# Kernel optimization log

Hardware: AMD Instinct MI355X
Metric: run time of the kernel (lower is better)

The kernel has to match this reference:

```python
import jax, jax.numpy as jnp
import numpy as np
from jax import lax

MIN_VALUE = 0.0
MAX_VALUE = 1.0

# 5-point Laplacian stencil kernel, OIHW layout
_LAP_KERNEL = jnp.array([[0.0, 1.0, 0.0],
                         [1.0, -4.0, 1.0],
                         [0.0, 1.0, 0.0]], dtype=jnp.float32).reshape(1, 1, 3, 3)


def _laplacian(u):
    # u: [B, 1, H, W], zero-padded 3x3 stencil (SAME)
    return lax.conv_general_dilated(
        u, _LAP_KERNEL, window_strides=(1, 1), padding='SAME',
        dimension_numbers=('NCHW', 'OIHW', 'NCHW'))


def _step(u, params):
    # Fisher-Kolmogorov reaction-diffusion step:
    #   diff = D * laplacian(u) + rho * u * (1 - u)
    D = params[:, 0:1]    # [B,1,H,W]
    rho = params[:, 1:2]  # [B,1,H,W]
    return D * _laplacian(u) + rho * u * (1.0 - u)


def setup_inputs() -> dict:
    key = jax.random.key(0)
    k1, k2, k3 = jax.random.split(key, 3)
    B, H, W = 32, 256, 256
    u = jax.random.uniform(k1, (B, 1, H, W), dtype=jnp.float32)
    params = jax.random.uniform(k2, (B, 2, H, W), dtype=jnp.float32)
    t = jax.random.randint(k3, (B,), 0, 32, dtype=jnp.int32)
    return {"u": u, "params": params, "t": t}


def reference(u, params, t):
    # Original: for step in range(max(t)): u[t>step] += step(u[t>step], params[t>step]); clip(u).
    # The step is per-sample local, so masked gather/scatter == predicated full update.
    max_duration = int(jnp.max(t))  # static trip count

    def body(step, u):
        mask = (t > step).astype(u.dtype)[:, None, None, None]  # [B,1,1,1]
        u = u + mask * _step(u, params)
        return jnp.clip(u, MIN_VALUE, MAX_VALUE)

    return lax.fori_loop(0, max_duration, body, u)
```

## Files before the change

### kernel.cpp

```cpp
#include <hip/hip_runtime.h>

#define HH 256
#define WW 256
#define PLANE (HH * WW)
#define CORE 32
#define HALO 16
#define SLAB 64
#define NW 16
#define RPW 4

__global__ __launch_bounds__(1024, 4)
void rd_tb16_kernel(const float* __restrict__ uin,
                    const float* __restrict__ params,
                    const int* __restrict__ t,
                    float* __restrict__ uout,
                    int base, int k)
{
    __shared__ float4 vt[2][NW][64];
    __shared__ float4 vb[2][NW][64];

    const int blk   = blockIdx.x;
    const int b     = blk >> 3;
    const int strip = blk & 7;
    const int r0    = strip * CORE;
    const int w     = threadIdx.x >> 6;
    const int lane  = threadIdx.x & 63;
    const int c0    = lane << 2;

    int ls = t[b] - base;
    ls = ls < 0 ? 0 : (ls > k ? k : ls);

    const int d_min = (w < 4) ? (13 - 4 * w) : ((w > 11) ? (4 * w - 47) : 0);
    int my_steps = ls - d_min;
    if (my_steps < 0) my_steps = 0;

    const int growbase = r0 - HALO + RPW * w;
    const size_t ubase = (size_t)b * PLANE;
    const size_t pbase = (size_t)b * 2 * PLANE;

    float u[RPW][4], pD[RPW][4], pR[RPW][4];

    #pragma unroll
    for (int dr = 0; dr < RPW; ++dr) {
        const int grow = growbase + dr;
        const bool inimg = (grow >= 0) && (grow < HH);
        int dist = 0;
        if (grow < r0)                 dist = r0 - grow;
        else if (grow > r0 + CORE - 1) dist = grow - (r0 + CORE - 1);
        const bool needU = inimg && (dist <= ls);
        const bool needP = inimg && (dist < ls);

        if (needU) {
            const float4 uu = *reinterpret_cast<const float4*>(uin + ubase + (size_t)grow * WW + c0);
            u[dr][0] = uu.x; u[dr][1] = uu.y; u[dr][2] = uu.z; u[dr][3] = uu.w;
        } else {
            u[dr][0] = u[dr][1] = u[dr][2] = u[dr][3] = 0.f;
        }
        if (needP) {
            const float4 dd = *reinterpret_cast<const float4*>(params + pbase + (size_t)grow * WW + c0);
            const float4 rr = *reinterpret_cast<const float4*>(params + pbase + PLANE + (size_t)grow * WW + c0);
            pD[dr][0] = dd.x; pD[dr][1] = dd.y; pD[dr][2] = dd.z; pD[dr][3] = dd.w;
            pR[dr][0] = rr.x; pR[dr][1] = rr.y; pR[dr][2] = rr.z; pR[dr][3] = rr.w;
        } else {
            pD[dr][0] = pD[dr][1] = pD[dr][2] = pD[dr][3] = 0.f;
            pR[dr][0] = pR[dr][1] = pR[dr][2] = pR[dr][3] = 0.f;
        }
    }

    if (ls > 0) {
        vt[0][w][lane] = make_float4(u[0][0], u[0][1], u[0][2], u[0][3]);
        vb[0][w][lane] = make_float4(u[RPW-1][0], u[RPW-1][1], u[RPW-1][2], u[RPW-1][3]);

        for (int s = 0; s < ls; ++s) {
            __syncthreads();
            if (s < my_steps) {
                const int cur = s & 1;

                float upr[4] = {0.f, 0.f, 0.f, 0.f};
                float dnr[4] = {0.f, 0.f, 0.f, 0.f};
                if (w > 0)      { float4 v = vb[cur][w-1][lane]; upr[0]=v.x; upr[1]=v.y; upr[2]=v.z; upr[3]=v.w; }
                if (w < NW - 1) { float4 v = vt[cur][w+1][lane]; dnr[0]=v.x; dnr[1]=v.y; dnr[2]=v.z; dnr[3]=v.w; }

                float nu[RPW][4];
                #pragma unroll
                for (int dr = 0; dr < RPW; ++dr) {
                    float lf = __shfl_up(u[dr][3], 1);
                    float rt = __shfl_down(u[dr][0], 1);
                    if (lane == 0)  lf = 0.f;
                    if (lane == 63) rt = 0.f;

                    #pragma unroll
                    for (int c = 0; c < 4; ++c) {
                        const float upv = dr ? u[dr-1][c] : upr[c];
                        const float dnv = (dr < RPW - 1) ? u[dr+1][c] : dnr[c];
                        const float lv  = c ? u[dr][c-1] : lf;
                        const float rv  = (c < 3) ? u[dr][c+1] : rt;
                        const float uc  = u[dr][c];
                        const float s4  = (upv + dnv) + (lv + rv);
                        const float lap = fmaf(-4.0f, uc, s4);
                        const float g   = fmaf(-uc, uc, uc);
                        const float a   = fmaf(pD[dr][c], lap, uc);
                        const float un  = fmaf(pR[dr][c], g, a);
                        nu[dr][c] = __builtin_amdgcn_fmed3f(un, 0.0f, 1.0f);
                    }
                }
                #pragma unroll
                for (int dr = 0; dr < RPW; ++dr)
                    #pragma unroll
                    for (int c = 0; c < 4; ++c)
                        u[dr][c] = nu[dr][c];

                const int nxt = cur ^ 1;
                vt[nxt][w][lane] = make_float4(u[0][0], u[0][1], u[0][2], u[0][3]);
                vb[nxt][w][lane] = make_float4(u[RPW-1][0], u[RPW-1][1], u[RPW-1][2], u[RPW-1][3]);
            }
        }
    }

    if (w >= HALO / RPW && w < (HALO + CORE) / RPW) {
        #pragma unroll
        for (int dr = 0; dr < RPW; ++dr) {
            const int grow = growbase + dr;
            *reinterpret_cast<float4*>(uout + ubase + (size_t)grow * WW + c0) =
                make_float4(u[dr][0], u[dr][1], u[dr][2], u[dr][3]);
        }
    }
}

extern "C" void kernel_launch(void* const* d_in, const int* in_sizes, int n_in,
                              void* d_out, int out_size, void* d_ws, size_t ws_size,
                              hipStream_t stream) {
    (void)in_sizes; (void)n_in; (void)out_size; (void)ws_size;
    const float* u      = (const float*)d_in[0];
    const float* params = (const float*)d_in[1];
    const int*   t      = (const int*)d_in[2];
    float*       out    = (float*)d_out;
    float*       ws     = (float*)d_ws;

    const dim3 grid(256), block(1024);
    rd_tb16_kernel<<<grid, block, 0, stream>>>(u,  params, t, ws,  0,  16);
    rd_tb16_kernel<<<grid, block, 0, stream>>>(ws, params, t, out, 16, 15);
}
```

Before: 52.58 us.

## Fuse two temporal-blocked launches into one deeper single-pass kernel

```diff
diff --git a/kernel.cpp b/kernel.cpp
--- a/kernel.cpp
+++ b/kernel.cpp
@@ -4,17 +4,15 @@
 #define WW 256
 #define PLANE (HH * WW)
 #define CORE 32
-#define HALO 16
-#define SLAB 64
+#define HALO 31
 #define NW 16
-#define RPW 4
+#define RPW 6
 
 __global__ __launch_bounds__(1024, 4)
-void rd_tb16_kernel(const float* __restrict__ uin,
-                    const float* __restrict__ params,
-                    const int* __restrict__ t,
-                    float* __restrict__ uout,
-                    int base, int k)
+void rd_single_kernel(const float* __restrict__ uin,
+                      const float* __restrict__ params,
+                      const int* __restrict__ t,
+                      float* __restrict__ uout)
 {
     __shared__ float4 vt[2][NW][64];
     __shared__ float4 vb[2][NW][64];
@@ -27,10 +25,14 @@
     const int lane  = threadIdx.x & 63;
     const int c0    = lane << 2;
 
-    int ls = t[b] - base;
-    ls = ls < 0 ? 0 : (ls > k ? k : ls);
+    int ls = t[b];
+    if (ls > 31) ls = 31;
+    if (ls < 0)  ls = 0;
 
-    const int d_min = (w < 4) ? (13 - 4 * w) : ((w > 11) ? (4 * w - 47) : 0);
+    int d_min;
+    if (w <= 4)       d_min = 26 - 6 * w;
+    else if (w >= 11) d_min = 6 * w - 62;
+    else              d_min = 0;
     int my_steps = ls - d_min;
     if (my_steps < 0) my_steps = 0;
 
@@ -81,7 +83,7 @@
                 if (w > 0)      { float4 v = vb[cur][w-1][lane]; upr[0]=v.x; upr[1]=v.y; upr[2]=v.z; upr[3]=v.w; }
                 if (w < NW - 1) { float4 v = vt[cur][w+1][lane]; dnr[0]=v.x; dnr[1]=v.y; dnr[2]=v.z; dnr[3]=v.w; }
 
-                float nu[RPW][4];
+                float up_old[4];
                 #pragma unroll
                 for (int dr = 0; dr < RPW; ++dr) {
                     float lf = __shfl_up(u[dr][3], 1);
@@ -89,26 +91,27 @@
                     if (lane == 0)  lf = 0.f;
                     if (lane == 63) rt = 0.f;
 
+                    float old[4], un[4];
+                    #pragma unroll
+                    for (int c = 0; c < 4; ++c) old[c] = u[dr][c];
+
                     #pragma unroll
                     for (int c = 0; c < 4; ++c) {
-                        const float upv = dr ? u[dr-1][c] : upr[c];
+                        const float upv = dr ? up_old[c] : upr[c];
                         const float dnv = (dr < RPW - 1) ? u[dr+1][c] : dnr[c];
-                        const float lv  = c ? u[dr][c-1] : lf;
-                        const float rv  = (c < 3) ? u[dr][c+1] : rt;
-                        const float uc  = u[dr][c];
+                        const float lv  = c ? old[c-1] : lf;
+                        const float rv  = (c < 3) ? old[c+1] : rt;
+                        const float uc  = old[c];
                         const float s4  = (upv + dnv) + (lv + rv);
                         const float lap = fmaf(-4.0f, uc, s4);
                         const float g   = fmaf(-uc, uc, uc);
                         const float a   = fmaf(pD[dr][c], lap, uc);
-                        const float un  = fmaf(pR[dr][c], g, a);
-                        nu[dr][c] = __builtin_amdgcn_fmed3f(un, 0.0f, 1.0f);
+                        const float nv  = fmaf(pR[dr][c], g, a);
+                        un[c] = __builtin_amdgcn_fmed3f(nv, 0.0f, 1.0f);
                     }
+                    #pragma unroll
+                    for (int c = 0; c < 4; ++c) { u[dr][c] = un[c]; up_old[c] = old[c]; }
                 }
-                #pragma unroll
-                for (int dr = 0; dr < RPW; ++dr)
-                    #pragma unroll
-                    for (int c = 0; c < 4; ++c)
-                        u[dr][c] = nu[dr][c];
 
                 const int nxt = cur ^ 1;
                 vt[nxt][w][lane] = make_float4(u[0][0], u[0][1], u[0][2], u[0][3]);
@@ -117,10 +120,10 @@
         }
     }
 
-    if (w >= HALO / RPW && w < (HALO + CORE) / RPW) {
-        #pragma unroll
-        for (int dr = 0; dr < RPW; ++dr) {
-            const int grow = growbase + dr;
+    #pragma unroll
+    for (int dr = 0; dr < RPW; ++dr) {
+        const int grow = growbase + dr;
+        if (grow >= r0 && grow < r0 + CORE) {
             *reinterpret_cast<float4*>(uout + ubase + (size_t)grow * WW + c0) =
                 make_float4(u[dr][0], u[dr][1], u[dr][2], u[dr][3]);
         }
@@ -130,14 +133,11 @@
 extern "C" void kernel_launch(void* const* d_in, const int* in_sizes, int n_in,
                               void* d_out, int out_size, void* d_ws, size_t ws_size,
                               hipStream_t stream) {
-    (void)in_sizes; (void)n_in; (void)out_size; (void)ws_size;
+    (void)in_sizes; (void)n_in; (void)out_size; (void)d_ws; (void)ws_size;
     const float* u      = (const float*)d_in[0];
     const float* params = (const float*)d_in[1];
     const int*   t      = (const int*)d_in[2];
     float*       out    = (float*)d_out;
-    float*       ws     = (float*)d_ws;
 
-    const dim3 grid(256), block(1024);
-    rd_tb16_kernel<<<grid, block, 0, stream>>>(u,  params, t, ws,  0,  16);
-    rd_tb16_kernel<<<grid, block, 0, stream>>>(ws, params, t, out, 16, 15);
+    rd_single_kernel<<<dim3(256), dim3(1024), 0, stream>>>(u, params, t, out);
 }
```

After: 52.50 us. No clear change (-0.1%).
